# Kernel optimization log

Measured on AMD Instinct MI355X. Metric: run time of the kernel, lower is better.

Reference implementation:

```python
import jax, jax.numpy as jnp
import numpy as np

B, SQ, SKV = 32, 200, 200
D, HEADS, L, V, FF = 1024, 16, 6, 32000, 2048
HD = D // HEADS
EPS = 1e-9


def _pe(seq_len, d):
    # sinusoidal positional encoding, matching PositionalEncoding
    pos = jnp.arange(seq_len, dtype=jnp.float32)[:, None]
    div = jnp.power(10000.0, jnp.arange(0, d, 2, dtype=jnp.float32) / d)
    ang = pos / div
    pe = jnp.zeros((seq_len, d), dtype=jnp.float32)
    pe = pe.at[:, 0::2].set(jnp.sin(ang))
    pe = pe.at[:, 1::2].set(jnp.cos(ang))
    return pe


def _ln(x, g, b):
    m = x.mean(-1, keepdims=True)
    v = ((x - m) ** 2).mean(-1, keepdims=True)  # unbiased=False
    return (x - m) / jnp.sqrt(v + EPS) * g + b


def _mha(xq, xk, xv, Wq, bq, Wk, bk, Wv, bv, Wo, mask):
    b, sq, _ = xq.shape
    sk = xk.shape[1]
    q = (xq @ Wq + bq).reshape(b, sq, HEADS, HD).transpose(0, 2, 1, 3)
    k = (xk @ Wk + bk).reshape(b, sk, HEADS, HD).transpose(0, 2, 1, 3)
    v = (xv @ Wv + bv).reshape(b, sk, HEADS, HD).transpose(0, 2, 1, 3)
    scores = jnp.einsum('bhqd,bhkd->bhqk', q, k) / jnp.float32(np.sqrt(HD))
    if mask is not None:
        scores = jnp.where(mask, -jnp.inf, scores)
    attn = jax.nn.softmax(scores, axis=-1)
    o = jnp.einsum('bhqk,bhkd->bhqd', attn, v).transpose(0, 2, 1, 3).reshape(b, sq, D)
    return o @ Wo


def setup_inputs() -> dict:
    key0 = jax.random.key(0)
    ks = list(jax.random.split(key0, 24))
    s = 0.02
    inp = {}
    # token ids in [1, V): avoid pad id 0 so no fully-masked softmax row (NaN)
    inp['query'] = jax.random.randint(ks[0], (B, SQ), 1, V)
    inp['key'] = jax.random.normal(ks[1], (B, SKV, D), jnp.float32)
    inp['value'] = jax.random.normal(ks[2], (B, SKV, D), jnp.float32)
    inp['emb'] = jax.random.normal(ks[3], (V, D), jnp.float32) * s
    for i, nm in enumerate(['ln1_g', 'ln2_g', 'ln3_g']):
        inp[nm] = jnp.ones((L, D), jnp.float32)
    for nm in ['ln1_b', 'ln2_b', 'ln3_b']:
        inp[nm] = jnp.zeros((L, D), jnp.float32)
    names = ['Wq_s', 'Wk_s', 'Wv_s', 'Wo_s', 'Wq_c', 'Wk_c', 'Wv_c', 'Wo_c']
    for i, nm in enumerate(names):
        inp[nm] = jax.random.normal(ks[4 + i], (L, D, D), jnp.float32) * s
    for nm in ['bq_s', 'bk_s', 'bv_s', 'bq_c', 'bk_c', 'bv_c']:
        inp[nm] = jnp.zeros((L, D), jnp.float32)
    inp['W1'] = jax.random.normal(ks[12], (L, D, FF), jnp.float32) * s
    inp['bf1'] = jnp.zeros((L, FF), jnp.float32)
    inp['W2'] = jax.random.normal(ks[13], (L, FF, D), jnp.float32) * s
    inp['bf2'] = jnp.zeros((L, D), jnp.float32)
    inp['lnf_g'] = jnp.ones((D,), jnp.float32)
    inp['lnf_b'] = jnp.zeros((D,), jnp.float32)
    return inp


def reference(query, key, value, emb, ln1_g, ln1_b, ln2_g, ln2_b, ln3_g, ln3_b,
              Wq_s, bq_s, Wk_s, bk_s, Wv_s, bv_s, Wo_s,
              Wq_c, bq_c, Wk_c, bk_c, Wv_c, bv_c, Wo_c,
              W1, bf1, W2, bf2, lnf_g, lnf_b):
    x = emb[query] + _pe(SQ, D)[None]  # dropout is identity at eval
    causal = jnp.triu(jnp.ones((SQ, SQ), dtype=bool), 1)[None, None]
    pad = (query == 0)[:, None, None, :]
    self_mask = causal | pad  # [B,1,SQ,SQ]
    o = x
    for l in range(L):
        qn = _ln(o, ln1_g[l], ln1_b[l])
        sa = _mha(qn, qn, qn, Wq_s[l], bq_s[l], Wk_s[l], bk_s[l], Wv_s[l], bv_s[l], Wo_s[l], self_mask)
        o1 = o + sa
        an = _ln(o1, ln2_g[l], ln2_b[l])
        ca = _mha(an, key, value, Wq_c[l], bq_c[l], Wk_c[l], bk_c[l], Wv_c[l], bv_c[l], Wo_c[l], None)
        o2 = o1 + ca
        cn = _ln(o2, ln3_g[l], ln3_b[l])
        ff = jax.nn.relu(cn @ W1[l] + bf1[l]) @ W2[l] + bf2[l]
        o = o2 + ff
    return _ln(o, lnf_g, lnf_b)
```

## Files before the change

kernel.cpp:

```cpp
#include <hip/hip_runtime.h>
#include <math.h>

#define BB  32
#define SQl 200
#define SKV 200
#define DD  1024
#define NH  16
#define HDm 64
#define NL  6
#define FFD 2048

typedef __attribute__((ext_vector_type(8))) short  short8v;
typedef __attribute__((ext_vector_type(4))) float  floatx4;

__device__ __forceinline__ ushort f2bf(float x) {
  uint u = __builtin_bit_cast(uint, x);
  u = (u + 0x7FFFu + ((u >> 16) & 1u)) >> 16;
  return (ushort)u;
}

__device__ __forceinline__ void gll16(const void* g, void* l) {
  __builtin_amdgcn_global_load_lds((const __attribute__((address_space(1))) void*)g,
                                   (__attribute__((address_space(3))) void*)l,
                                   16, 0, 0);
}

__global__ __launch_bounds__(256) void embed_pe_kernel(const int* __restrict__ qids,
                                                       const float* __restrict__ emb,
                                                       float* __restrict__ x) {
  int idx = blockIdx.x * 256 + threadIdx.x;
  int d   = idx & (DD - 1);
  int row = idx >> 10;
  int s   = row % SQl;
  int tok = qids[row];
  float expo = (float)(d & ~1) * (1.0f / (float)DD);
  float dv   = powf(10000.0f, expo);
  float ang  = (float)s / dv;
  float pe   = (d & 1) ? cosf(ang) : sinf(ang);
  x[idx] = emb[(size_t)tok * DD + d] + pe;
}

__global__ __launch_bounds__(256) void cvt_bf16_kernel(const float* __restrict__ in,
                                                       ushort* __restrict__ out, int n8) {
  int idx = blockIdx.x * 256 + threadIdx.x;
  if (idx >= n8) return;
  const floatx4 va = ((const floatx4*)in)[idx * 2];
  const floatx4 vb = ((const floatx4*)in)[idx * 2 + 1];
  short8v o;
  o[0] = (short)f2bf(va.x); o[1] = (short)f2bf(va.y);
  o[2] = (short)f2bf(va.z); o[3] = (short)f2bf(va.w);
  o[4] = (short)f2bf(vb.x); o[5] = (short)f2bf(vb.y);
  o[6] = (short)f2bf(vb.z); o[7] = (short)f2bf(vb.w);
  ((short8v*)out)[idx] = o;
}

struct P8 { const float* p[8]; };
__global__ __launch_bounds__(256) void transpose48_kernel(P8 srcs, ushort* __restrict__ dst) {
  __shared__ float t[32][33];
  const size_t MEL = (size_t)DD * DD;
  const int z = blockIdx.z;
  const int arr = z / 6, l = z - arr * 6;
  const size_t base[8] = {0, MEL, 2*MEL, 18*MEL, 24*MEL, 30*MEL, 36*MEL, 42*MEL};
  const size_t lstr[8] = {3*MEL, 3*MEL, 3*MEL, MEL, MEL, MEL, MEL, MEL};
  const float* __restrict__ W = srcs.p[arr] + (size_t)l * MEL;
  ushort* __restrict__ WT = dst + base[arr] + (size_t)l * lstr[arr];
  const int n0 = blockIdx.x * 32, k0 = blockIdx.y * 32;
  const int tx = threadIdx.x & 31, ty = threadIdx.x >> 5;
#pragma unroll
  for (int i = 0; i < 4; ++i)
    t[ty + i * 8][tx] = W[(size_t)(k0 + ty + i * 8) * DD + n0 + tx];
  __syncthreads();
#pragma unroll
  for (int i = 0; i < 4; ++i)
    WT[(size_t)(n0 + ty + i * 8) * DD + k0 + tx] = f2bf(t[tx][ty + i * 8]);
}

__global__ __launch_bounds__(256) void transposeW_kernel(const float* __restrict__ src,
                                                         ushort* __restrict__ dst,
                                                         int K, int N) {
  __shared__ float t[32][33];
  const int z = blockIdx.z;
  const float* __restrict__ W = src + (size_t)z * K * N;
  ushort* __restrict__ WT = dst + (size_t)z * K * N;
  const int n0 = blockIdx.x * 32, k0 = blockIdx.y * 32;
  const int tx = threadIdx.x & 31, ty = threadIdx.x >> 5;
#pragma unroll
  for (int i = 0; i < 4; ++i)
    t[ty + i * 8][tx] = W[(size_t)(k0 + ty + i * 8) * N + n0 + tx];
  __syncthreads();
#pragma unroll
  for (int i = 0; i < 4; ++i)
    WT[(size_t)(n0 + ty + i * 8) * K + k0 + tx] = f2bf(t[tx][ty + i * 8]);
}

template <int OBF16>
__global__ __launch_bounds__(256) void ln4_kernel(const float* __restrict__ in,
                                                  const float* __restrict__ gam,
                                                  const float* __restrict__ bet,
                                                  float* __restrict__ outf,
                                                  ushort* __restrict__ outb) {
  const int wid  = threadIdx.x >> 6;
  const int lane = threadIdx.x & 63;
  const int row  = blockIdx.x * 4 + wid;
  const float* ip = in + (size_t)row * DD;

  float4 x[4];
  float s = 0.f, sq = 0.f;
#pragma unroll
  for (int i = 0; i < 4; ++i) {
    x[i] = *(const float4*)&ip[i * 256 + lane * 4];
    s  += x[i].x + x[i].y + x[i].z + x[i].w;
    sq += x[i].x * x[i].x + x[i].y * x[i].y + x[i].z * x[i].z + x[i].w * x[i].w;
  }
#pragma unroll
  for (int msk = 1; msk < 64; msk <<= 1) {
    s  += __shfl_xor(s,  msk, 64);
    sq += __shfl_xor(sq, msk, 64);
  }
  const float m   = s * (1.0f / (float)DD);
  const float var = sq * (1.0f / (float)DD) - m * m;
  const float inv = rsqrtf(var + 1e-9f);

#pragma unroll
  for (int i = 0; i < 4; ++i) {
    const int c = i * 256 + lane * 4;
    const float4 g4 = *(const float4*)&gam[c];
    const float4 b4 = *(const float4*)&bet[c];
    float o0 = (x[i].x - m) * inv * g4.x + b4.x;
    float o1 = (x[i].y - m) * inv * g4.y + b4.y;
    float o2 = (x[i].z - m) * inv * g4.z + b4.z;
    float o3 = (x[i].w - m) * inv * g4.w + b4.w;
    if (OBF16) {
      uint2 pk;
      pk.x = (uint)f2bf(o0) | ((uint)f2bf(o1) << 16);
      pk.y = (uint)f2bf(o2) | ((uint)f2bf(o3) << 16);
      *(uint2*)&outb[(size_t)row * DD + c] = pk;
    } else {
      float4 ov; ov.x = o0; ov.y = o1; ov.z = o2; ov.w = o3;
      *(float4*)&outf[(size_t)row * DD + c] = ov;
    }
  }
}

struct BiasP { const float* p[6]; };

template <int RELU, int ACC, int OBF16, int NT>
__global__ __launch_bounds__(256) void gemm128_mfma(const ushort* __restrict__ A,
                                                    const ushort* __restrict__ BT,
                                                    BiasP bias,
                                                    float* __restrict__ C,
                                                    ushort* __restrict__ Cb,
                                                    int ldc) {
  constexpr int K = NT * 64;
  __shared__ short8v As[1024];
  __shared__ short8v Bs[1024];
  const int tid  = threadIdx.x;
  const int wid  = tid >> 6;
  const int lane = tid & 63;

  const int nwg = gridDim.x * gridDim.y;
  int wg = blockIdx.y * gridDim.x + blockIdx.x;
  wg = (wg & 7) * (nwg >> 3) + (wg >> 3);
  const int bn = (wg % gridDim.x) * 128;
  const int bm = (wg / gridDim.x) * 128;

  const int wm = (wid >> 1) * 64;
  const int wn = (wid & 1) * 64;
  const int lq = lane & 15;
  const int lg = lane >> 4;

  const ushort* aS[4];
  const ushort* bS[4];
#pragma unroll
  for (int i = 0; i < 4; ++i) {
    const int s   = i * 256 + wid * 64 + lane;
    const int row = s >> 3;
    const int kg  = (s & 7) ^ (row & 7);
    aS[i] = A  + (size_t)(bm + row) * K + kg * 8;
    bS[i] = BT + (size_t)(bn + row) * K + kg * 8;
  }

  int aIdx[4], bIdx[4];
#pragma unroll
  for (int i = 0; i < 4; ++i) {
    const int mr = wm + i * 16 + lq;
    aIdx[i] = mr * 8 + (lg ^ (mr & 7));
    const int nr = wn + i * 16 + lq;
    bIdx[i] = nr * 8 + (lg ^ (nr & 7));
  }

  floatx4 acc[4][4];
  const floatx4 fz = {0.f, 0.f, 0.f, 0.f};
#pragma unroll
  for (int mi = 0; mi < 4; ++mi)
#pragma unroll
    for (int ni = 0; ni < 4; ++ni) acc[mi][ni] = fz;

#pragma unroll
  for (int t = 0; t < NT; ++t) {
    const int ko = t * 64;
#pragma unroll
    for (int i = 0; i < 4; ++i) gll16(aS[i] + ko, &As[i * 256 + wid * 64]);
#pragma unroll
    for (int i = 0; i < 4; ++i) gll16(bS[i] + ko, &Bs[i * 256 + wid * 64]);
    __syncthreads();
#pragma unroll
    for (int kk = 0; kk < 2; ++kk) {
      short8v af[4], bf_[4];
#pragma unroll
      for (int i = 0; i < 4; ++i) {
        af[i]  = As[aIdx[i] ^ (kk * 4)];
        bf_[i] = Bs[bIdx[i] ^ (kk * 4)];
      }
#pragma unroll
      for (int mi = 0; mi < 4; ++mi)
#pragma unroll
        for (int ni = 0; ni < 4; ++ni)
          acc[mi][ni] = __builtin_amdgcn_mfma_f32_16x16x32_bf16(af[mi], bf_[ni], acc[mi][ni], 0, 0, 0);
    }
    __syncthreads();
  }

#pragma unroll
  for (int mi = 0; mi < 4; ++mi) {
    const int row = bm + wm + mi * 16 + lg * 4;
#pragma unroll
    for (int ni = 0; ni < 4; ++ni) {
      const int col = bn + wn + ni * 16 + lq;
      const float* bp = bias.p[col >> 10];
      const float bvv = bp ? bp[col & (DD - 1)] : 0.f;
#pragma unroll
      for (int r = 0; r < 4; ++r) {
        float val = acc[mi][ni][r] + bvv;
        if (ACC)  val += C[(size_t)(row + r) * ldc + col];
        if (RELU) val = fmaxf(val, 0.f);
        if (OBF16) Cb[(size_t)(row + r) * ldc + col] = f2bf(val);
        else       C [(size_t)(row + r) * ldc + col] = val;
      }
    }
  }
}

static inline void launch_g(const ushort* A, const ushort* BT, BiasP bias,
                            float* C, ushort* Cb, int M, int N, int K, int ldc,
                            int mode, hipStream_t s) {
  dim3 grid(N / 128, M / 128), blk(256);
  if (K == 2048) {
    gemm128_mfma<0, 1, 0, 32><<<grid, blk, 0, s>>>(A, BT, bias, C, Cb, ldc);
  } else if (mode == 1) {
    gemm128_mfma<0, 1, 0, 16><<<grid, blk, 0, s>>>(A, BT, bias, C, Cb, ldc);
  } else if (mode == 2) {
    gemm128_mfma<1, 0, 1, 16><<<grid, blk, 0, s>>>(A, BT, bias, C, Cb, ldc);
  } else {
    gemm128_mfma<0, 0, 1, 16><<<grid, blk, 0, s>>>(A, BT, bias, C, Cb, ldc);
  }
}

template <int CAUSAL>
__global__ __launch_bounds__(256, 2) void attn_mfma_kernel(const ushort* __restrict__ q, int qs,
                                                           const ushort* __restrict__ k, int ks,
                                                           const ushort* __restrict__ v, int vs,
                                                           const int* __restrict__ qids,
                                                           ushort* __restrict__ out) {
  __shared__ short8v Kl[208 * 8];
  __shared__ ushort  Vt[64 * 256];
  __shared__ short8v Pl[1024];
  __shared__ float   padf[224];

  const int bh   = blockIdx.x;
  const int h    = bh & (NH - 1);
  const int b    = bh >> 4;
  const int tid  = threadIdx.x;
  const int w    = tid >> 6;
  const int lane = tid & 63;
  const int lq   = lane & 15;
  const int lg   = lane >> 4;

  if (tid < 208) {
    const int kp = tid;
    if (kp < SKV) {
      const short8v* src = (const short8v*)(k + ((size_t)(b * SKV + kp)) * ks + h * HDm);
#pragma unroll
      for (int s = 0; s < 8; ++s) Kl[kp * 8 + (s ^ (kp & 7))] = src[s];
    } else {
      const short8v z = {0, 0, 0, 0, 0, 0, 0, 0};
#pragma unroll
      for (int s = 0; s < 8; ++s) Kl[kp * 8 + s] = z;
    }
  }
  if (tid < 224) {
    const int kp = tid;
    float pf = 1.f;
    if (kp < SKV) {
      pf = CAUSAL ? ((qids[b * SQl + kp] == 0) ? 1.f : 0.f) : 0.f;
      const short8v* src = (const short8v*)(v + ((size_t)(b * SKV + kp)) * vs + h * HDm);
      const int s3 = kp >> 3, k7 = kp & 7;
#pragma unroll
      for (int li = 0; li < 8; ++li) {
        const short8v vv = src[li];
#pragma unroll
        for (int e = 0; e < 8; ++e)
          Vt[(li * 8 + e) * 256 + ((s3 ^ e) * 8) + k7] = (ushort)vv[e];
      }
    } else {
      const int s3 = kp >> 3, k7 = kp & 7;
#pragma unroll
      for (int li = 0; li < 8; ++li)
#pragma unroll
        for (int e = 0; e < 8; ++e)
          Vt[(li * 8 + e) * 256 + ((s3 ^ e) * 8) + k7] = 0;
    }
    padf[kp] = pf;
  }
  __syncthreads();

  short8v qf[4][2];
#pragma unroll
  for (int i = 0; i < 4; ++i) {
    const int mt = i * 4 + w;
    if (mt > 12) continue;
    int qrow = mt * 16 + lq;
    if (qrow > SQl - 1) qrow = SQl - 1;
    const ushort* qp = q + ((size_t)(b * SQl + qrow)) * qs + h * HDm + lg * 8;
    qf[i][0] = *(const short8v*)qp;
    qf[i][1] = *(const short8v*)(qp + 32);
  }

  float rmax[4][4];
#pragma unroll
  for (int i = 0; i < 4; ++i)
#pragma unroll
    for (int r = 0; r < 4; ++r) rmax[i][r] = -3e38f;

  for (int kt = 0; kt < 13; ++kt) {
    const int kp = kt * 16 + lq;
    const short8v bk0 = Kl[kp * 8 + (lg ^ (kp & 7))];
    const short8v bk1 = Kl[kp * 8 + ((4 + lg) ^ (kp & 7))];
    const float pmask = padf[kp];
#pragma unroll
    for (int i = 0; i < 4; ++i) {
      const int mt = i * 4 + w;
      if (mt > 12) continue;
      floatx4 S = {0.f, 0.f, 0.f, 0.f};
      S = __builtin_amdgcn_mfma_f32_16x16x32_bf16(qf[i][0], bk0, S, 0, 0, 0);
      S = __builtin_amdgcn_mfma_f32_16x16x32_bf16(qf[i][1], bk1, S, 0, 0, 0);
#pragma unroll
      for (int r = 0; r < 4; ++r) {
        const int qrow = mt * 16 + lg * 4 + r;
        bool masked = (pmask != 0.f);
        if (CAUSAL) masked = masked || (kp > qrow);
        const float s = masked ? -3e38f : S[r] * 0.125f;
        rmax[i][r] = fmaxf(rmax[i][r], s);
      }
    }
  }
#pragma unroll
  for (int msk = 1; msk < 16; msk <<= 1)
#pragma unroll
    for (int i = 0; i < 4; ++i)
#pragma unroll
      for (int r = 0; r < 4; ++r)
        rmax[i][r] = fmaxf(rmax[i][r], __shfl_xor(rmax[i][r], msk, 64));

  float rsum[4][4];
  floatx4 Of[4][4];
  const floatx4 fz = {0.f, 0.f, 0.f, 0.f};
#pragma unroll
  for (int i = 0; i < 4; ++i)
#pragma unroll
    for (int r = 0; r < 4; ++r) { rsum[i][r] = 0.f; Of[i][r] = fz; }

  for (int kc = 0; kc < 7; ++kc) {
#pragma unroll
    for (int t = 0; t < 2; ++t) {
      const int kt = kc * 2 + t;
      const int kp = kt * 16 + lq;
      short8v bk0, bk1;
      float pmask = 1.f;
      if (kt < 13) {
        bk0 = Kl[kp * 8 + (lg ^ (kp & 7))];
        bk1 = Kl[kp * 8 + ((4 + lg) ^ (kp & 7))];
        pmask = padf[kp];
      }
#pragma unroll
      for (int i = 0; i < 4; ++i) {
        const int mt = i * 4 + w;
        if (mt > 12) continue;
        floatx4 S = {0.f, 0.f, 0.f, 0.f};
        if (kt < 13) {
          S = __builtin_amdgcn_mfma_f32_16x16x32_bf16(qf[i][0], bk0, S, 0, 0, 0);
          S = __builtin_amdgcn_mfma_f32_16x16x32_bf16(qf[i][1], bk1, S, 0, 0, 0);
        }
#pragma unroll
        for (int r = 0; r < 4; ++r) {
          const int qrow = mt * 16 + lg * 4 + r;
          bool masked = (kt >= 13) || (pmask != 0.f);
          if (CAUSAL) masked = masked || (kp > qrow);
          const float p = masked ? 0.f : __expf(S[r] * 0.125f - rmax[i][r]);
          rsum[i][r] += p;
          const int qrl  = lg * 4 + r;
          const int kpl  = t * 16 + lq;
          const int slot = (kpl >> 3) ^ ((qrl >> 2) & 3);
          ((ushort*)Pl)[(w * 4 + i) * 512 + qrl * 32 + slot * 8 + (kpl & 7)] = f2bf(p);
        }
      }
    }
    short8v vb[4];
#pragma unroll
    for (int dt = 0; dt < 4; ++dt) {
      const int d  = dt * 16 + lq;
      const int sk = kc * 4 + lg;
      vb[dt] = ((const short8v*)Vt)[d * 32 + (sk ^ (d & 7))];
    }
#pragma unroll
    for (int i = 0; i < 4; ++i) {
      const int mt = i * 4 + w;
      if (mt > 12) continue;
      const short8v pa = Pl[(w * 4 + i) * 64 + lq * 4 + (lg ^ ((lq >> 2) & 3))];
#pragma unroll
      for (int dt = 0; dt < 4; ++dt)
        Of[i][dt] = __builtin_amdgcn_mfma_f32_16x16x32_bf16(pa, vb[dt], Of[i][dt], 0, 0, 0);
    }
  }

#pragma unroll
  for (int msk = 1; msk < 16; msk <<= 1)
#pragma unroll
    for (int i = 0; i < 4; ++i)
#pragma unroll
      for (int r = 0; r < 4; ++r)
        rsum[i][r] += __shfl_xor(rsum[i][r], msk, 64);

#pragma unroll
  for (int i = 0; i < 4; ++i) {
    const int mt = i * 4 + w;
    if (mt > 12) continue;
#pragma unroll
    for (int r = 0; r < 4; ++r) {
      const int qrow = mt * 16 + lg * 4 + r;
      if (qrow >= SQl) continue;
      const float linv = 1.0f / rsum[i][r];
      ushort* op = out + ((size_t)(b * SQl + qrow)) * DD + h * HDm;
#pragma unroll
      for (int dt = 0; dt < 4; ++dt)
        op[dt * 16 + lq] = f2bf(Of[i][dt][r] * linv);
    }
  }
}

extern "C" void kernel_launch(void* const* d_in, const int* in_sizes, int n_in,
                              void* d_out, int out_size, void* d_ws, size_t ws_size,
                              hipStream_t stream) {
  (void)in_sizes; (void)n_in; (void)out_size; (void)ws_size;

  const int*   qids  = (const int*)  d_in[0];
  const float* key   = (const float*)d_in[1];
  const float* value = (const float*)d_in[2];
  const float* emb   = (const float*)d_in[3];
  const float* ln1_g = (const float*)d_in[4];
  const float* ln2_g = (const float*)d_in[5];
  const float* ln3_g = (const float*)d_in[6];
  const float* ln1_b = (const float*)d_in[7];
  const float* ln2_b = (const float*)d_in[8];
  const float* ln3_b = (const float*)d_in[9];
  const float* Wq_s  = (const float*)d_in[10];
  const float* Wk_s  = (const float*)d_in[11];
  const float* Wv_s  = (const float*)d_in[12];
  const float* Wo_s  = (const float*)d_in[13];
  const float* Wq_c  = (const float*)d_in[14];
  const float* Wk_c  = (const float*)d_in[15];
  const float* Wv_c  = (const float*)d_in[16];
  const float* Wo_c  = (const float*)d_in[17];
  const float* bq_s  = (const float*)d_in[18];
  const float* bk_s  = (const float*)d_in[19];
  const float* bv_s  = (const float*)d_in[20];
  const float* bq_c  = (const float*)d_in[21];
  const float* bk_c  = (const float*)d_in[22];
  const float* bv_c  = (const float*)d_in[23];
  const float* W1    = (const float*)d_in[24];
  const float* bf1   = (const float*)d_in[25];
  const float* W2    = (const float*)d_in[26];
  const float* bf2   = (const float*)d_in[27];
  const float* lnf_g = (const float*)d_in[28];
  const float* lnf_b = (const float*)d_in[29];

  const size_t NTOK = (size_t)BB * SQl * DD;
  const size_t MEL  = (size_t)DD * DD;
  char* w = (char*)d_ws;
  float*  o    = (float*)w;  w += NTOK * 4;
  ushort* t0b  = (ushort*)w; w += NTOK * 2;
  ushort* qkv  = (ushort*)w; w += (size_t)BB * SQl * 3 * DD * 2;
  ushort* kc   = (ushort*)w; w += (size_t)BB * SQl * 6 * DD * 2;
  ushort* vc   = (ushort*)w; w += (size_t)BB * SQl * 6 * DD * 2;
  ushort* kb   = (ushort*)w; w += NTOK * 2;
  ushort* vb   = (ushort*)w; w += NTOK * 2;
  ushort* fbb  = (ushort*)w; w += (size_t)BB * SQl * FFD * 2;
  ushort* wt   = (ushort*)w; w += 48 * MEL * 2;
  ushort* wt1  = (ushort*)w; w += (size_t)NL * DD * FFD * 2;
  ushort* wt2  = (ushort*)w; w += (size_t)NL * FFD * DD * 2;

  const int M = BB * SQl;
  const BiasP nob = {{nullptr, nullptr, nullptr, nullptr, nullptr, nullptr}};

  embed_pe_kernel<<<(int)(NTOK / 256), 256, 0, stream>>>(qids, emb, o);
  cvt_bf16_kernel<<<(int)(NTOK / 8 + 255) / 256, 256, 0, stream>>>(key,   kb, (int)(NTOK / 8));
  cvt_bf16_kernel<<<(int)(NTOK / 8 + 255) / 256, 256, 0, stream>>>(value, vb, (int)(NTOK / 8));

  P8 p8 = {{Wq_s, Wk_s, Wv_s, Wo_s, Wq_c, Wk_c, Wv_c, Wo_c}};
  transpose48_kernel<<<dim3(32, 32, 48), 256, 0, stream>>>(p8, wt);
  transposeW_kernel<<<dim3(FFD / 32, DD / 32, NL), 256, 0, stream>>>(W1, wt1, DD, FFD);
  transposeW_kernel<<<dim3(DD / 32, FFD / 32, NL), 256, 0, stream>>>(W2, wt2, FFD, DD);

  ushort* wtQKV = wt;
  ushort* wtOs  = wt + 18 * MEL;
  ushort* wtQc  = wt + 24 * MEL;
  ushort* wtKc  = wt + 30 * MEL;
  ushort* wtVc  = wt + 36 * MEL;
  ushort* wtOc  = wt + 42 * MEL;

  {
    BiasP bk6, bv6;
#pragma unroll
    for (int l = 0; l < NL; ++l) { bk6.p[l] = bk_c + l * DD; bv6.p[l] = bv_c + l * DD; }
    launch_g(kb, wtKc, bk6, nullptr, kc, M, 6 * DD, DD, 6 * DD, 3, stream);
    launch_g(vb, wtVc, bv6, nullptr, vc, M, 6 * DD, DD, 6 * DD, 3, stream);
  }

  for (int l = 0; l < NL; ++l) {
    ln4_kernel<1><<<M / 4, 256, 0, stream>>>(o, ln1_g + l * DD, ln1_b + l * DD, nullptr, t0b);
    BiasP bqkv = {{bq_s + l * DD, bk_s + l * DD, bv_s + l * DD, nullptr, nullptr, nullptr}};
    launch_g(t0b, wtQKV + l * 3 * MEL, bqkv, nullptr, qkv, M, 3 * DD, DD, 3 * DD, 3, stream);
    attn_mfma_kernel<1><<<BB * NH, 256, 0, stream>>>(qkv, 3 * DD, qkv + DD, 3 * DD,
                                                     qkv + 2 * DD, 3 * DD, qids, t0b);
    launch_g(t0b, wtOs + l * MEL, nob, o, nullptr, M, DD, DD, DD, 1, stream);

    ln4_kernel<1><<<M / 4, 256, 0, stream>>>(o, ln2_g + l * DD, ln2_b + l * DD, nullptr, t0b);
    BiasP bqc = {{bq_c + l * DD, nullptr, nullptr, nullptr, nullptr, nullptr}};
    launch_g(t0b, wtQc + l * MEL, bqc, nullptr, qkv, M, DD, DD, 3 * DD, 3, stream);
    attn_mfma_kernel<0><<<BB * NH, 256, 0, stream>>>(qkv, 3 * DD, kc + l * DD, 6 * DD,
                                                     vc + l * DD, 6 * DD, nullptr, t0b);
    launch_g(t0b, wtOc + l * MEL, nob, o, nullptr, M, DD, DD, DD, 1, stream);

    ln4_kernel<1><<<M / 4, 256, 0, stream>>>(o, ln3_g + l * DD, ln3_b + l * DD, nullptr, t0b);
    BiasP bf1p = {{bf1 + l * FFD, bf1 + l * FFD + DD, nullptr, nullptr, nullptr, nullptr}};
    launch_g(t0b, wt1 + (size_t)l * DD * FFD, bf1p, nullptr, fbb, M, FFD, DD, FFD, 2, stream);
    BiasP bf2p = {{bf2 + l * DD, nullptr, nullptr, nullptr, nullptr, nullptr}};
    launch_g(fbb, wt2 + (size_t)l * FFD * DD, bf2p, o, nullptr, M, DD, FFD, DD, 1, stream);
  }

  ln4_kernel<0><<<M / 4, 256, 0, stream>>>(o, lnf_g, lnf_b, (float*)d_out, nullptr);
}
```

Measured before the change: 2.382 ms.

## Overlap next-tile global-to-LDS loads with MFMA compute in GEMM

Restructures the GEMM main loop so each K tile is read fully from LDS into registers, then the next tile's global-to-LDS loads are issued before the MFMAs run. This hides global load latency behind compute within a single LDS buffer, using explicit waitcnt, barriers and sched_barrier. It also raises wave priority around the MFMA block and drops the XCD-aware workgroup remapping in favour of plain block indexing. That could reduce L2 locality across chiplets and adds register pressure from holding both k-halves of the fragments.

Result: slower. 2.538 ms (+6.5%).

```diff
diff --git a/kernel.cpp b/kernel.cpp
--- a/kernel.cpp
+++ b/kernel.cpp
@@ -12,6 +12,11 @@
 
 typedef __attribute__((ext_vector_type(8))) short  short8v;
 typedef __attribute__((ext_vector_type(4))) float  floatx4;
+
+#define SBAR()   asm volatile("s_barrier" ::: "memory")
+#define VMCNT0() asm volatile("s_waitcnt vmcnt(0)" ::: "memory")
+#define LGKM0()  asm volatile("s_waitcnt lgkmcnt(0)" ::: "memory")
+#define SCHEDB() __builtin_amdgcn_sched_barrier(0)
 
 __device__ __forceinline__ ushort f2bf(float x) {
   uint u = __builtin_bit_cast(uint, x);
@@ -157,13 +162,8 @@
   const int tid  = threadIdx.x;
   const int wid  = tid >> 6;
   const int lane = tid & 63;
-
-  const int nwg = gridDim.x * gridDim.y;
-  int wg = blockIdx.y * gridDim.x + blockIdx.x;
-  wg = (wg & 7) * (nwg >> 3) + (wg >> 3);
-  const int bn = (wg % gridDim.x) * 128;
-  const int bm = (wg / gridDim.x) * 128;
-
+  const int bm = blockIdx.y * 128;
+  const int bn = blockIdx.x * 128;
   const int wm = (wid >> 1) * 64;
   const int wn = (wid & 1) * 64;
   const int lq = lane & 15;
@@ -197,28 +197,45 @@
     for (int ni = 0; ni < 4; ++ni) acc[mi][ni] = fz;
 
 #pragma unroll
+  for (int i = 0; i < 4; ++i) gll16(aS[i], &As[i * 256 + wid * 64]);
+#pragma unroll
+  for (int i = 0; i < 4; ++i) gll16(bS[i], &Bs[i * 256 + wid * 64]);
+  VMCNT0();
+  SBAR(); SCHEDB();
+
+#pragma unroll
   for (int t = 0; t < NT; ++t) {
-    const int ko = t * 64;
-#pragma unroll
-    for (int i = 0; i < 4; ++i) gll16(aS[i] + ko, &As[i * 256 + wid * 64]);
-#pragma unroll
-    for (int i = 0; i < 4; ++i) gll16(bS[i] + ko, &Bs[i * 256 + wid * 64]);
-    __syncthreads();
-#pragma unroll
-    for (int kk = 0; kk < 2; ++kk) {
-      short8v af[4], bf_[4];
+    short8v af[2][4], bf_[2][4];
+#pragma unroll
+    for (int kk = 0; kk < 2; ++kk)
 #pragma unroll
       for (int i = 0; i < 4; ++i) {
-        af[i]  = As[aIdx[i] ^ (kk * 4)];
-        bf_[i] = Bs[bIdx[i] ^ (kk * 4)];
+        af[kk][i]  = As[aIdx[i] ^ (kk * 4)];
+        bf_[kk][i] = Bs[bIdx[i] ^ (kk * 4)];
       }
+    LGKM0(); SCHEDB();
+    SBAR(); SCHEDB();
+
+    if (t + 1 < NT) {
+      const int ko = (t + 1) * 64;
+#pragma unroll
+      for (int i = 0; i < 4; ++i) gll16(aS[i] + ko, &As[i * 256 + wid * 64]);
+#pragma unroll
+      for (int i = 0; i < 4; ++i) gll16(bS[i] + ko, &Bs[i * 256 + wid * 64]);
+    }
+
+    __builtin_amdgcn_s_setprio(1);
+#pragma unroll
+    for (int kk = 0; kk < 2; ++kk)
 #pragma unroll
       for (int mi = 0; mi < 4; ++mi)
 #pragma unroll
         for (int ni = 0; ni < 4; ++ni)
-          acc[mi][ni] = __builtin_amdgcn_mfma_f32_16x16x32_bf16(af[mi], bf_[ni], acc[mi][ni], 0, 0, 0);
-    }
-    __syncthreads();
+          acc[mi][ni] = __builtin_amdgcn_mfma_f32_16x16x32_bf16(af[kk][mi], bf_[kk][ni], acc[mi][ni], 0, 0, 0);
+    __builtin_amdgcn_s_setprio(0);
+
+    if (t + 1 < NT) { VMCNT0(); }
+    SBAR(); SCHEDB();
   }
 
 #pragma unroll
```

## Replace two-pass attention softmax with online softmax using lazy rescaling

Applied to the files above, without the earlier changes.

Removes the separate max-finding pass over all key tiles, which recomputed QK^T MFMAs, and switches to an online softmax. The running max is only raised when a new score exceeds it by more than a threshold of 8, and a wave-wide vote skips the rescale otherwise. This roughly halves the QK^T MFMA work in the attention kernel. In exchange it keeps more score registers live, adds cross-lane shuffles whenever a rescale fires, and lets exponentials reach up to e^8 before renormalising.

New measurement: 2.384 ms. Within noise of the previous version (+0.1%).

```diff
diff --git a/kernel.cpp b/kernel.cpp
--- a/kernel.cpp
+++ b/kernel.cpp
@@ -326,51 +326,16 @@
     qf[i][1] = *(const short8v*)(qp + 32);
   }
 
-  float rmax[4][4];
-#pragma unroll
-  for (int i = 0; i < 4; ++i)
-#pragma unroll
-    for (int r = 0; r < 4; ++r) rmax[i][r] = -3e38f;
-
-  for (int kt = 0; kt < 13; ++kt) {
-    const int kp = kt * 16 + lq;
-    const short8v bk0 = Kl[kp * 8 + (lg ^ (kp & 7))];
-    const short8v bk1 = Kl[kp * 8 + ((4 + lg) ^ (kp & 7))];
-    const float pmask = padf[kp];
-#pragma unroll
-    for (int i = 0; i < 4; ++i) {
-      const int mt = i * 4 + w;
-      if (mt > 12) continue;
-      floatx4 S = {0.f, 0.f, 0.f, 0.f};
-      S = __builtin_amdgcn_mfma_f32_16x16x32_bf16(qf[i][0], bk0, S, 0, 0, 0);
-      S = __builtin_amdgcn_mfma_f32_16x16x32_bf16(qf[i][1], bk1, S, 0, 0, 0);
-#pragma unroll
-      for (int r = 0; r < 4; ++r) {
-        const int qrow = mt * 16 + lg * 4 + r;
-        bool masked = (pmask != 0.f);
-        if (CAUSAL) masked = masked || (kp > qrow);
-        const float s = masked ? -3e38f : S[r] * 0.125f;
-        rmax[i][r] = fmaxf(rmax[i][r], s);
-      }
-    }
-  }
-#pragma unroll
-  for (int msk = 1; msk < 16; msk <<= 1)
-#pragma unroll
-    for (int i = 0; i < 4; ++i)
-#pragma unroll
-      for (int r = 0; r < 4; ++r)
-        rmax[i][r] = fmaxf(rmax[i][r], __shfl_xor(rmax[i][r], msk, 64));
-
-  float rsum[4][4];
+  float m_[4][4], rsum[4][4];
   floatx4 Of[4][4];
   const floatx4 fz = {0.f, 0.f, 0.f, 0.f};
 #pragma unroll
   for (int i = 0; i < 4; ++i)
 #pragma unroll
-    for (int r = 0; r < 4; ++r) { rsum[i][r] = 0.f; Of[i][r] = fz; }
+    for (int r = 0; r < 4; ++r) { m_[i][r] = -3e38f; rsum[i][r] = 0.f; Of[i][r] = fz; }
 
   for (int kc = 0; kc < 7; ++kc) {
+    floatx4 sv[2][4];
 #pragma unroll
     for (int t = 0; t < 2; ++t) {
       const int kt = kc * 2 + t;
@@ -385,18 +350,57 @@
 #pragma unroll
       for (int i = 0; i < 4; ++i) {
         const int mt = i * 4 + w;
-        if (mt > 12) continue;
         floatx4 S = {0.f, 0.f, 0.f, 0.f};
-        if (kt < 13) {
+        if (kt < 13 && mt <= 12) {
           S = __builtin_amdgcn_mfma_f32_16x16x32_bf16(qf[i][0], bk0, S, 0, 0, 0);
           S = __builtin_amdgcn_mfma_f32_16x16x32_bf16(qf[i][1], bk1, S, 0, 0, 0);
         }
 #pragma unroll
         for (int r = 0; r < 4; ++r) {
           const int qrow = mt * 16 + lg * 4 + r;
-          bool masked = (kt >= 13) || (pmask != 0.f);
+          bool masked = (kt >= 13) || (mt > 12) || (pmask != 0.f);
           if (CAUSAL) masked = masked || (kp > qrow);
-          const float p = masked ? 0.f : __expf(S[r] * 0.125f - rmax[i][r]);
+          sv[t][i][r] = masked ? -3e38f : S[r] * 0.125f;
+        }
+      }
+    }
+
+    bool trig = false;
+#pragma unroll
+    for (int t = 0; t < 2; ++t)
+#pragma unroll
+      for (int i = 0; i < 4; ++i)
+#pragma unroll
+        for (int r = 0; r < 4; ++r)
+          trig = trig || (sv[t][i][r] > m_[i][r] + 8.f);
+    if (__any(trig)) {
+#pragma unroll
+      for (int i = 0; i < 4; ++i)
+#pragma unroll
+        for (int r = 0; r < 4; ++r) {
+          float tm = fmaxf(sv[0][i][r], sv[1][i][r]);
+#pragma unroll
+          for (int msk = 1; msk < 16; msk <<= 1)
+            tm = fmaxf(tm, __shfl_xor(tm, msk, 64));
+          const float mn = fmaxf(m_[i][r], tm);
+          const float sc = __expf(m_[i][r] - mn);
+          rsum[i][r] *= sc;
+#pragma unroll
+          for (int dt = 0; dt < 4; ++dt) Of[i][dt][r] *= sc;
+          m_[i][r] = mn;
+        }
+    }
+
+#pragma unroll
+    for (int t = 0; t < 2; ++t)
+#pragma unroll
+      for (int i = 0; i < 4; ++i) {
+        const int mt = i * 4 + w;
+        if (mt > 12) continue;
+#pragma unroll
+        for (int r = 0; r < 4; ++r) {
+          const float s = sv[t][i][r];
+          const float p = (s < -1e37f) ? 0.f : __expf(s - m_[i][r]);
           rsum[i][r] += p;
           const int qrl  = lg * 4 + r;
           const int kpl  = t * 16 + lq;
@@ -404,7 +408,7 @@
           ((ushort*)Pl)[(w * 4 + i) * 512 + qrl * 32 + slot * 8 + (kpl & 7)] = f2bf(p);
         }
       }
-    }
+
     short8v vb[4];
 #pragma unroll
     for (int dt = 0; dt < 4; ++dt) {
```
